# Kernel tuning notes

Hardware: AMD Instinct MI355X
Metric: run time of the kernel (lower is better)

The kernel has to match this reference:

```python
import jax, jax.numpy as jnp
import numpy as np

N, F, H = 22, 448, 64
LN_EPS = 1e-5


def _layernorm(h, g, b):
    mu = h.mean(axis=-1, keepdims=True)
    var = ((h - mu) ** 2).mean(axis=-1, keepdims=True)
    return (h - mu) / jnp.sqrt(var + LN_EPS) * g + b


def setup_inputs() -> dict:
    key = jax.random.key(0)
    ks = jax.random.split(key, 16)
    B = 128
    x = jax.random.normal(ks[0], (B, N, F), dtype=jnp.float32)
    s = lambda fan_in: 1.0 / np.sqrt(fan_in)
    # correlation-branch edge_weight_net: Linear(2F,64) -> ReLU -> Linear(64,1) -> Sigmoid
    cw1 = jax.random.uniform(ks[1], (2 * F, 64), jnp.float32, -s(2 * F), s(2 * F))
    cb1 = jax.random.uniform(ks[2], (64,), jnp.float32, -s(2 * F), s(2 * F))
    cw2 = jax.random.uniform(ks[3], (64, 1), jnp.float32, -s(64), s(64))
    cb2 = jax.random.uniform(ks[4], (1,), jnp.float32, -s(64), s(64))
    # semantic branch
    emb = jax.random.normal(ks[5], (N, H), dtype=jnp.float32) * 0.01
    D = 2 * H + 2 * F
    sw1 = jax.random.uniform(ks[6], (D, H), jnp.float32, -s(D), s(D))
    sb1 = jax.random.uniform(ks[7], (H,), jnp.float32, -s(D), s(D))
    ln_g = jnp.ones((H,), jnp.float32)
    ln_b = jnp.zeros((H,), jnp.float32)
    sw2 = jax.random.uniform(ks[8], (H, H // 2), jnp.float32, -s(H), s(H))
    sb2 = jax.random.uniform(ks[9], (H // 2,), jnp.float32, -s(H), s(H))
    sw3 = jax.random.uniform(ks[10], (H // 2, 1), jnp.float32, -s(H // 2), s(H // 2))
    sb3 = jax.random.uniform(ks[11], (1,), jnp.float32, -s(H // 2), s(H // 2))
    thr = jnp.asarray(0.3, jnp.float32)
    alpha_p = jnp.asarray(0.6, jnp.float32)
    return dict(x=x, cw1=cw1, cb1=cb1, cw2=cw2, cb2=cb2, emb=emb,
                sw1=sw1, sb1=sb1, ln_g=ln_g, ln_b=ln_b,
                sw2=sw2, sb2=sb2, sw3=sw3, sb3=sb3,
                thr=thr, alpha_p=alpha_p)


def reference(x, cw1, cb1, cw2, cb2, emb, sw1, sb1, ln_g, ln_b,
              sw2, sb2, sw3, sb3, thr, alpha_p):
    B, n, f = x.shape
    eye = jnp.eye(n, dtype=x.dtype)[None]

    # ---- Correlation graph ----
    xc = x - x.mean(axis=-1, keepdims=True)
    std = jnp.std(x, axis=-1, ddof=1, keepdims=True) + 1e-8  # torch std is unbiased
    xn = xc / std
    corr = jnp.abs(jnp.einsum('bif,bjf->bij', xn, xn) / f)
    # pairwise edge features (B,N,N,2F)
    xi = jnp.broadcast_to(x[:, :, None, :], (B, n, n, f))
    xj = jnp.broadcast_to(x[:, None, :, :], (B, n, n, f))
    ef = jnp.concatenate([xi, xj], axis=-1)
    h = jax.nn.relu(ef @ cw1 + cb1)
    w_corr = jax.nn.sigmoid((h @ cw2 + cb2)[..., 0])
    g_corr = corr * w_corr + eye

    # ---- Semantic graph ----
    ei = jnp.broadcast_to(emb[None, :, None, :], (B, n, n, H))
    ej = jnp.broadcast_to(emb[None, None, :, :], (B, n, n, H))
    sf = jnp.concatenate([ei, ej, xi, xj], axis=-1)  # (B,N,N,2H+2F)
    h1 = jax.nn.relu(_layernorm(sf @ sw1 + sb1, ln_g, ln_b))
    h2 = jax.nn.relu(h1 @ sw2 + sb2)
    w_sem = jax.nn.sigmoid((h2 @ sw3 + sb3)[..., 0])  # (B,N,N)
    # original loop fills only i<j and mirrors; diagonal stays 0
    upper = jnp.triu(w_sem, k=1)
    adj = upper + jnp.swapaxes(upper, 1, 2)
    t = jax.nn.sigmoid(thr)
    adj = jnp.where(adj > t, adj, jnp.zeros_like(adj))
    g_sem = adj + eye

    # ---- Learned fusion ----
    alpha = jax.nn.sigmoid(alpha_p)
    return alpha * g_corr + (1.0 - alpha) * g_sem
```

## Files before the change

kernel.cpp:

```cpp
#include <hip/hip_runtime.h>
#include <math.h>

namespace {
constexpr int kN = 22;
constexpr int kF = 448;
constexpr int kNP = kN * kN;
constexpr int kXStr = 452;
constexpr int kSm1 = kN * kXStr + 2 * kN;
constexpr int kAStr = 68;
constexpr int kBStr = 68;
constexpr int kPStr = 68;
constexpr int kVStr = 68;
}

__global__ __launch_bounds__(256) void hgc_k1(
    const float* __restrict__ x,
    const float* __restrict__ cw1, const float* __restrict__ cb1,
    const float* __restrict__ emb,
    const float* __restrict__ sw1, const float* __restrict__ sb1,
    float* __restrict__ C, float* __restrict__ g,
    int M, int Mtiles, int nGemm)
{
    __shared__ __align__(16) float sm[kSm1];
    const int tid = threadIdx.x;

    if ((int)blockIdx.x < nGemm) {
        float* As = sm;
        float* Bs = sm + 64 * kAStr;
        const int bm = blockIdx.x % Mtiles;
        const int bn = blockIdx.x / Mtiles;
        const int m0 = bm * 64;

        const float* Wsrc =
            (bn == 0) ? cw1 :
            (bn == 1) ? cw1 + 448 * 64 :
            (bn == 2) ? sw1 + 128 * 64 :
                        sw1 + 576 * 64;

        const int tm = tid & 15;
        const int tn = tid >> 4;
        const int ld_row = tid >> 4;
        const int ld_kq  = tid & 15;

        float acc[4][4];
        #pragma unroll
        for (int i = 0; i < 4; ++i)
            #pragma unroll
            for (int j = 0; j < 4; ++j) acc[i][j] = 0.f;

        float4 rA[4], rB[4];
        #pragma unroll
        for (int p = 0; p < 4; ++p) {
            const int row = ld_row + p * 16;
            int m = m0 + row; if (m >= M) m = M - 1;
            rA[p] = *(const float4*)&x[(size_t)m * kF + ld_kq * 4];
            rB[p] = *(const float4*)&Wsrc[(size_t)row * 64 + ld_kq * 4];
        }

        for (int k0 = 0; k0 < kF; k0 += 64) {
            #pragma unroll
            for (int p = 0; p < 4; ++p) {
                const int row = ld_row + p * 16;
                As[(ld_kq * 4 + 0) * kAStr + row] = rA[p].x;
                As[(ld_kq * 4 + 1) * kAStr + row] = rA[p].y;
                As[(ld_kq * 4 + 2) * kAStr + row] = rA[p].z;
                As[(ld_kq * 4 + 3) * kAStr + row] = rA[p].w;
                *(float4*)&Bs[row * kBStr + ld_kq * 4] = rB[p];
            }
            __syncthreads();
            const int kn = k0 + 64;
            if (kn < kF) {
                #pragma unroll
                for (int p = 0; p < 4; ++p) {
                    const int row = ld_row + p * 16;
                    int m = m0 + row; if (m >= M) m = M - 1;
                    rA[p] = *(const float4*)&x[(size_t)m * kF + kn + ld_kq * 4];
                    rB[p] = *(const float4*)&Wsrc[(size_t)(kn + row) * 64 + ld_kq * 4];
                }
            } else if (bn >= 2) {
                const float* W2 = sw1 + (bn == 2 ? 0 : 64) * 64;
                #pragma unroll
                for (int p = 0; p < 4; ++p) {
                    const int row = ld_row + p * 16;
                    const int r = (m0 + row) % kN;
                    rA[p] = *(const float4*)&emb[(size_t)r * 64 + ld_kq * 4];
                    rB[p] = *(const float4*)&W2[(size_t)row * 64 + ld_kq * 4];
                }
            }
            #pragma unroll 8
            for (int k = 0; k < 64; ++k) {
                const float4 a4 = *(const float4*)&As[k * kAStr + tm * 4];
                const float4 b4 = *(const float4*)&Bs[k * kBStr + tn * 4];
                acc[0][0] = fmaf(a4.x, b4.x, acc[0][0]); acc[0][1] = fmaf(a4.x, b4.y, acc[0][1]);
                acc[0][2] = fmaf(a4.x, b4.z, acc[0][2]); acc[0][3] = fmaf(a4.x, b4.w, acc[0][3]);
                acc[1][0] = fmaf(a4.y, b4.x, acc[1][0]); acc[1][1] = fmaf(a4.y, b4.y, acc[1][1]);
                acc[1][2] = fmaf(a4.y, b4.z, acc[1][2]); acc[1][3] = fmaf(a4.y, b4.w, acc[1][3]);
                acc[2][0] = fmaf(a4.z, b4.x, acc[2][0]); acc[2][1] = fmaf(a4.z, b4.y, acc[2][1]);
                acc[2][2] = fmaf(a4.z, b4.z, acc[2][2]); acc[2][3] = fmaf(a4.z, b4.w, acc[2][3]);
                acc[3][0] = fmaf(a4.w, b4.x, acc[3][0]); acc[3][1] = fmaf(a4.w, b4.y, acc[3][1]);
                acc[3][2] = fmaf(a4.w, b4.z, acc[3][2]); acc[3][3] = fmaf(a4.w, b4.w, acc[3][3]);
            }
            __syncthreads();
        }

        if (bn >= 2) {
            #pragma unroll
            for (int p = 0; p < 4; ++p) {
                const int row = ld_row + p * 16;
                As[(ld_kq * 4 + 0) * kAStr + row] = rA[p].x;
                As[(ld_kq * 4 + 1) * kAStr + row] = rA[p].y;
                As[(ld_kq * 4 + 2) * kAStr + row] = rA[p].z;
                As[(ld_kq * 4 + 3) * kAStr + row] = rA[p].w;
                *(float4*)&Bs[row * kBStr + ld_kq * 4] = rB[p];
            }
            __syncthreads();
            #pragma unroll 8
            for (int k = 0; k < 64; ++k) {
                const float4 a4 = *(const float4*)&As[k * kAStr + tm * 4];
                const float4 b4 = *(const float4*)&Bs[k * kBStr + tn * 4];
                acc[0][0] = fmaf(a4.x, b4.x, acc[0][0]); acc[0][1] = fmaf(a4.x, b4.y, acc[0][1]);
                acc[0][2] = fmaf(a4.x, b4.z, acc[0][2]); acc[0][3] = fmaf(a4.x, b4.w, acc[0][3]);
                acc[1][0] = fmaf(a4.y, b4.x, acc[1][0]); acc[1][1] = fmaf(a4.y, b4.y, acc[1][1]);
                acc[1][2] = fmaf(a4.y, b4.z, acc[1][2]); acc[1][3] = fmaf(a4.y, b4.w, acc[1][3]);
                acc[2][0] = fmaf(a4.z, b4.x, acc[2][0]); acc[2][1] = fmaf(a4.z, b4.y, acc[2][1]);
                acc[2][2] = fmaf(a4.z, b4.z, acc[2][2]); acc[2][3] = fmaf(a4.z, b4.w, acc[2][3]);
                acc[3][0] = fmaf(a4.w, b4.x, acc[3][0]); acc[3][1] = fmaf(a4.w, b4.y, acc[3][1]);
                acc[3][2] = fmaf(a4.w, b4.z, acc[3][2]); acc[3][3] = fmaf(a4.w, b4.w, acc[3][3]);
            }
        }

        float4 bias = {0, 0, 0, 0};
        if (bn == 0)      bias = *(const float4*)&cb1[tn * 4];
        else if (bn == 2) bias = *(const float4*)&sb1[tn * 4];
        #pragma unroll
        for (int i = 0; i < 4; ++i) {
            const int m = m0 + tm * 4 + i;
            if (m < M) {
                float4 o;
                o.x = acc[i][0] + bias.x; o.y = acc[i][1] + bias.y;
                o.z = acc[i][2] + bias.z; o.w = acc[i][3] + bias.w;
                *(float4*)&C[(size_t)m * 256 + bn * 64 + tn * 4] = o;
            }
        }
    } else {
        float* smu = sm + kN * kXStr;
        float* sis = smu + kN;
        const int b = blockIdx.x - nGemm;

        const float4* xb4 = (const float4*)(x + (size_t)b * (kN * kF));
        for (int idx = tid; idx < kN * kF / 4; idx += 256) {
            const float4 v = xb4[idx];
            const int r = idx / 112;
            const int k = (idx - r * 112) * 4;
            float* d = sm + r * kXStr + k;
            d[0] = v.x; d[1] = v.y; d[2] = v.z; d[3] = v.w;
        }
        __syncthreads();

        {
            const int wid = tid >> 6, lane = tid & 63;
            for (int r = wid; r < kN; r += 4) {
                const float* row = sm + r * kXStr;
                float s = 0.f;
                #pragma unroll
                for (int c = 0; c < 7; ++c) s += row[c * 64 + lane];
                #pragma unroll
                for (int o = 32; o; o >>= 1) s += __shfl_xor(s, o, 64);
                const float mean = s * (1.f / 448.f);
                float ss = 0.f;
                #pragma unroll
                for (int c = 0; c < 7; ++c) { const float d = row[c * 64 + lane] - mean; ss = fmaf(d, d, ss); }
                #pragma unroll
                for (int o = 32; o; o >>= 1) ss += __shfl_xor(ss, o, 64);
                if (lane == 0) {
                    smu[r] = mean;
                    sis[r] = 1.f / (sqrtf(ss * (1.f / 447.f)) + 1e-8f);
                }
            }
        }
        __syncthreads();

        if (tid < 253) {
            int rem = tid, i = 0;
            while (rem >= kN - i) { rem -= kN - i; ++i; }
            const int j = i + rem;
            const float4* ri = (const float4*)(sm + i * kXStr);
            const float4* rj = (const float4*)(sm + j * kXStr);
            float dot = 0.f;
            for (int q = 0; q < 112; ++q) {
                const float4 a = ri[q], bq = rj[q];
                dot = fmaf(a.x, bq.x, dot); dot = fmaf(a.y, bq.y, dot);
                dot = fmaf(a.z, bq.z, dot); dot = fmaf(a.w, bq.w, dot);
            }
            const float c = (dot - 448.f * smu[i] * smu[j]) * sis[i] * sis[j] * (1.f / 448.f);
            const float ac = fabsf(c);
            g[(size_t)b * kNP + i * 22 + j] = ac;
            g[(size_t)b * kNP + j * 22 + i] = ac;
        }
    }
}

__global__ __launch_bounds__(256) void hgc_k2(
    const float* __restrict__ C, const float* __restrict__ g,
    const float* __restrict__ cw2, const float* __restrict__ cb2,
    const float* __restrict__ sw2, const float* __restrict__ sb2,
    const float* __restrict__ sw3, const float* __restrict__ sb3,
    const float* __restrict__ ln_g, const float* __restrict__ ln_b,
    const float* __restrict__ thr, const float* __restrict__ alpha_p,
    float* __restrict__ out)
{
    __shared__ __align__(16) float sp[4 * kN * kPStr];
    __shared__ float sg[kNP];
    __shared__ __align__(16) float sw2s[2048];
    __shared__ float scw2[64], slng[64], slnb[64], ssw3[32], ssb2[32];
    __shared__ __align__(16) float vbuf[32 * kVStr];

    const int tid = threadIdx.x;
    const int b   = blockIdx.x >> 1;
    const int pb  = blockIdx.x & 1;

    #pragma unroll
    for (int a = 0; a < 4; ++a) {
        float* dst = sp + a * kN * kPStr;
        for (int idx = tid; idx < 352; idx += 256) {
            const int r = idx >> 4, kq = idx & 15;
            const float4 v = *(const float4*)&C[((size_t)(b * 22 + r)) * 256 + a * 64 + kq * 4];
            *(float4*)&dst[r * kPStr + kq * 4] = v;
        }
    }
    for (int idx = tid; idx < kNP; idx += 256) sg[idx] = g[(size_t)b * kNP + idx];
    {
        const float4* s4 = (const float4*)sw2;
        for (int idx = tid; idx < 512; idx += 256)
            *((float4*)(sw2s + idx * 4)) = s4[idx];
    }
    if (tid < 64)       { scw2[tid] = cw2[tid]; slng[tid] = ln_g[tid]; slnb[tid] = ln_b[tid]; }
    else if (tid < 96)  { ssw3[tid - 64] = sw3[tid - 64]; }
    else if (tid < 128) { ssb2[tid - 96] = sb2[tid - 96]; }
    __syncthreads();

    const int pl = tid >> 3;
    const int t  = tid & 7;
    const float* sa1 = sp;
    const float* sa2 = sp + kN * kPStr;
    const float* su1 = sp + 2 * kN * kPStr;
    const float* su2 = sp + 3 * kN * kPStr;

    for (int ch = 0; ch < 4; ++ch) {
        const int s_  = pb * 128 + ch * 32 + pl;
        const bool valid = s_ < 253;
        const int s = valid ? s_ : 252;
        int i, j;
        if (s < 231) {
            int rem = s, i0 = 0;
            while (rem >= 21 - i0) { rem -= 21 - i0; ++i0; }
            i = i0; j = i0 + 1 + rem;
        } else { i = j = s - 231; }

        float zc1 = 0.f, zc2 = 0.f;
        {
            const float* a1i = sa1 + i * kPStr + t * 8;
            const float* a2j = sa2 + j * kPStr + t * 8;
            const float* a1j = sa1 + j * kPStr + t * 8;
            const float* a2i = sa2 + i * kPStr + t * 8;
            const float4 i0 = *(const float4*)a1i, i1 = *(const float4*)(a1i + 4);
            const float4 j0 = *(const float4*)a2j, j1 = *(const float4*)(a2j + 4);
            const float4 k0 = *(const float4*)a1j, k1 = *(const float4*)(a1j + 4);
            const float4 l0 = *(const float4*)a2i, l1 = *(const float4*)(a2i + 4);
            const float4 w0 = *(const float4*)(scw2 + t * 8);
            const float4 w1 = *(const float4*)(scw2 + t * 8 + 4);
            zc1 = fmaf(fmaxf(i0.x + j0.x, 0.f), w0.x, zc1);
            zc1 = fmaf(fmaxf(i0.y + j0.y, 0.f), w0.y, zc1);
            zc1 = fmaf(fmaxf(i0.z + j0.z, 0.f), w0.z, zc1);
            zc1 = fmaf(fmaxf(i0.w + j0.w, 0.f), w0.w, zc1);
            zc1 = fmaf(fmaxf(i1.x + j1.x, 0.f), w1.x, zc1);
            zc1 = fmaf(fmaxf(i1.y + j1.y, 0.f), w1.y, zc1);
            zc1 = fmaf(fmaxf(i1.z + j1.z, 0.f), w1.z, zc1);
            zc1 = fmaf(fmaxf(i1.w + j1.w, 0.f), w1.w, zc1);
            zc2 = fmaf(fmaxf(k0.x + l0.x, 0.f), w0.x, zc2);
            zc2 = fmaf(fmaxf(k0.y + l0.y, 0.f), w0.y, zc2);
            zc2 = fmaf(fmaxf(k0.z + l0.z, 0.f), w0.z, zc2);
            zc2 = fmaf(fmaxf(k0.w + l0.w, 0.f), w0.w, zc2);
            zc2 = fmaf(fmaxf(k1.x + l1.x, 0.f), w1.x, zc2);
            zc2 = fmaf(fmaxf(k1.y + l1.y, 0.f), w1.y, zc2);
            zc2 = fmaf(fmaxf(k1.z + l1.z, 0.f), w1.z, zc2);
            zc2 = fmaf(fmaxf(k1.w + l1.w, 0.f), w1.w, zc2);
            zc1 += __shfl_xor(zc1, 1, 64); zc1 += __shfl_xor(zc1, 2, 64); zc1 += __shfl_xor(zc1, 4, 64);
            zc2 += __shfl_xor(zc2, 1, 64); zc2 += __shfl_xor(zc2, 2, 64); zc2 += __shfl_xor(zc2, 4, 64);
        }

        float raw[8];
        float s1 = 0.f;
        {
            const float* pu1 = su1 + i * kPStr + t * 8;
            const float* pu2 = su2 + j * kPStr + t * 8;
            const float4 u0 = *(const float4*)pu1, u1v = *(const float4*)(pu1 + 4);
            const float4 v0 = *(const float4*)pu2, v1v = *(const float4*)(pu2 + 4);
            raw[0] = u0.x + v0.x; raw[1] = u0.y + v0.y; raw[2] = u0.z + v0.z; raw[3] = u0.w + v0.w;
            raw[4] = u1v.x + v1v.x; raw[5] = u1v.y + v1v.y; raw[6] = u1v.z + v1v.z; raw[7] = u1v.w + v1v.w;
            #pragma unroll
            for (int c = 0; c < 8; ++c) s1 += raw[c];
        }
        s1 += __shfl_xor(s1, 1, 64); s1 += __shfl_xor(s1, 2, 64); s1 += __shfl_xor(s1, 4, 64);
        const float mean = s1 * (1.f / 64.f);
        float s2 = 0.f;
        #pragma unroll
        for (int c = 0; c < 8; ++c) { const float d = raw[c] - mean; s2 = fmaf(d, d, s2); }
        s2 += __shfl_xor(s2, 1, 64); s2 += __shfl_xor(s2, 2, 64); s2 += __shfl_xor(s2, 4, 64);
        const float rstd = rsqrtf(s2 * (1.f / 64.f) + 1e-5f);
        {
            float* vb = vbuf + pl * kVStr + t * 8;
            float4 o0, o1;
            o0.x = fmaxf(fmaf((raw[0] - mean) * rstd, slng[t*8+0], slnb[t*8+0]), 0.f);
            o0.y = fmaxf(fmaf((raw[1] - mean) * rstd, slng[t*8+1], slnb[t*8+1]), 0.f);
            o0.z = fmaxf(fmaf((raw[2] - mean) * rstd, slng[t*8+2], slnb[t*8+2]), 0.f);
            o0.w = fmaxf(fmaf((raw[3] - mean) * rstd, slng[t*8+3], slnb[t*8+3]), 0.f);
            o1.x = fmaxf(fmaf((raw[4] - mean) * rstd, slng[t*8+4], slnb[t*8+4]), 0.f);
            o1.y = fmaxf(fmaf((raw[5] - mean) * rstd, slng[t*8+5], slnb[t*8+5]), 0.f);
            o1.z = fmaxf(fmaf((raw[6] - mean) * rstd, slng[t*8+6], slnb[t*8+6]), 0.f);
            o1.w = fmaxf(fmaf((raw[7] - mean) * rstd, slng[t*8+7], slnb[t*8+7]), 0.f);
            *(float4*)vb = o0;
            *(float4*)(vb + 4) = o1;
        }
        __syncthreads();

        float4 acc = {0, 0, 0, 0};
        {
            const float* vb = vbuf + pl * kVStr;
            for (int k = 0; k < 64; ++k) {
                const float v = vb[k];
                const float4 w = *((const float4*)(sw2s + k * 32 + t * 4));
                acc.x = fmaf(v, w.x, acc.x); acc.y = fmaf(v, w.y, acc.y);
                acc.z = fmaf(v, w.z, acc.z); acc.w = fmaf(v, w.w, acc.w);
            }
        }
        float z2;
        {
            const int o0 = t * 4;
            z2  = fmaxf(acc.x + ssb2[o0 + 0], 0.f) * ssw3[o0 + 0];
            z2 += fmaxf(acc.y + ssb2[o0 + 1], 0.f) * ssw3[o0 + 1];
            z2 += fmaxf(acc.z + ssb2[o0 + 2], 0.f) * ssw3[o0 + 2];
            z2 += fmaxf(acc.w + ssb2[o0 + 3], 0.f) * ssw3[o0 + 3];
            z2 += __shfl_xor(z2, 1, 64); z2 += __shfl_xor(z2, 2, 64); z2 += __shfl_xor(z2, 4, 64);
        }

        if (valid && t == 0) {
            const float alpha = 1.f / (1.f + __expf(-alpha_p[0]));
            const float wc_ij = 1.f / (1.f + __expf(-(zc1 + cb2[0])));
            float gsem;
            if (i == j) {
                gsem = 1.f;
            } else {
                const float wsem = 1.f / (1.f + expf(-(z2 + sb3[0])));
                const float tt   = 1.f / (1.f + expf(-thr[0]));
                gsem = (wsem > tt) ? wsem : 0.f;
            }
            const float gc_ij = fmaf(sg[i * 22 + j], wc_ij, (i == j) ? 1.f : 0.f);
            out[(size_t)b * kNP + i * 22 + j] = fmaf(alpha, gc_ij, (1.f - alpha) * gsem);
            if (i != j) {
                const float wc_ji = 1.f / (1.f + __expf(-(zc2 + cb2[0])));
                const float gc_ji = sg[j * 22 + i] * wc_ji;
                out[(size_t)b * kNP + j * 22 + i] = fmaf(alpha, gc_ji, (1.f - alpha) * gsem);
            }
        }
        __syncthreads();
    }
}

extern "C" void kernel_launch(void* const* d_in, const int* in_sizes, int n_in,
                              void* d_out, int out_size, void* d_ws, size_t ws_size,
                              hipStream_t stream)
{
    (void)n_in; (void)out_size; (void)ws_size;
    const float* x     = (const float*)d_in[0];
    const float* cw1   = (const float*)d_in[1];
    const float* cb1   = (const float*)d_in[2];
    const float* cw2   = (const float*)d_in[3];
    const float* cb2   = (const float*)d_in[4];
    const float* emb   = (const float*)d_in[5];
    const float* sw1   = (const float*)d_in[6];
    const float* sb1   = (const float*)d_in[7];
    const float* ln_g  = (const float*)d_in[8];
    const float* ln_b  = (const float*)d_in[9];
    const float* sw2   = (const float*)d_in[10];
    const float* sb2   = (const float*)d_in[11];
    const float* sw3   = (const float*)d_in[12];
    const float* sb3   = (const float*)d_in[13];
    const float* thr   = (const float*)d_in[14];
    const float* alpha = (const float*)d_in[15];
    float* out = (float*)d_out;
    float* ws  = (float*)d_ws;

    const int B = in_sizes[0] / (kN * kF);
    const int M = kN * B;
    const int Mtiles = (M + 63) / 64;
    const int nGemm = Mtiles * 4;

    float* C = ws;
    float* g = ws + (size_t)M * 256;

    hipLaunchKernelGGL(hgc_k1, dim3(nGemm + B), dim3(256), 0, stream,
                       x, cw1, cb1, emb, sw1, sb1, C, g, M, Mtiles, nGemm);
    hipLaunchKernelGGL(hgc_k2, dim3(2 * B), dim3(256), 0, stream,
                       C, g, cw2, cb2, sw2, sb2, sw3, sb3, ln_g, ln_b, thr, alpha, out);
}
```

Before: 135.1 us.

## Halve GEMM tile rows and split corr and pair kernels across more blocks

The GEMM tile in the first kernel shrinks from 64 to 32 rows, so each thread computes 2x4 outputs and twice as many blocks are launched. The correlation branch is split into two blocks per batch, each handling 11 rows and computing every (i,j) entry directly instead of mirroring. The second kernel is split into four blocks per batch, each processing two chunks of pairs. The aim is more blocks to fill the GPU's compute units, at the cost of less data reuse per tile, repeated loading of x in the correlation blocks, and duplicated dot products.

```diff
diff --git a/kernel.cpp b/kernel.cpp
--- a/kernel.cpp
+++ b/kernel.cpp
@@ -4,13 +4,23 @@
 namespace {
 constexpr int kN = 22;
 constexpr int kF = 448;
-constexpr int kNP = kN * kN;
+constexpr int kNP = 484;
 constexpr int kXStr = 452;
 constexpr int kSm1 = kN * kXStr + 2 * kN;
-constexpr int kAStr = 68;
+constexpr int kAStr = 36;
 constexpr int kBStr = 68;
 constexpr int kPStr = 68;
 constexpr int kVStr = 68;
+
+__device__ __forceinline__ void map_slot(int s, int& i, int& j) {
+    if (s < 231) {
+        int rem = s, i0 = 0;
+        while (rem >= 21 - i0) { rem -= 21 - i0; ++i0; }
+        i = i0; j = i0 + 1 + rem;
+    } else {
+        i = j = s - 231;
+    }
+}
 }
 
 __global__ __launch_bounds__(256) void hgc_k1(
@@ -29,7 +39,7 @@
         float* Bs = sm + 64 * kAStr;
         const int bm = blockIdx.x % Mtiles;
         const int bn = blockIdx.x / Mtiles;
-        const int m0 = bm * 64;
+        const int m0 = bm * 32;
 
         const float* Wsrc =
             (bn == 0) ? cw1 :
@@ -39,102 +49,99 @@
 
         const int tm = tid & 15;
         const int tn = tid >> 4;
-        const int ld_row = tid >> 4;
-        const int ld_kq  = tid & 15;
-
-        float acc[4][4];
+        float acc[2][4];
         #pragma unroll
-        for (int i = 0; i < 4; ++i)
+        for (int i = 0; i < 2; ++i)
             #pragma unroll
             for (int j = 0; j < 4; ++j) acc[i][j] = 0.f;
 
-        float4 rA[4], rB[4];
-        #pragma unroll
-        for (int p = 0; p < 4; ++p) {
-            const int row = ld_row + p * 16;
-            int m = m0 + row; if (m >= M) m = M - 1;
-            rA[p] = *(const float4*)&x[(size_t)m * kF + ld_kq * 4];
-            rB[p] = *(const float4*)&Wsrc[(size_t)row * 64 + ld_kq * 4];
-        }
-
-        for (int k0 = 0; k0 < kF; k0 += 64) {
+        float4 rA[2], rB[4];
+
+        auto preMain = [&](int k0) {
+            #pragma unroll
+            for (int p = 0; p < 2; ++p) {
+                const int idx = tid + p * 256;
+                const int row = idx >> 4, kq = idx & 15;
+                int m = m0 + row; if (m >= M) m = M - 1;
+                rA[p] = *(const float4*)&x[(size_t)m * kF + k0 + kq * 4];
+            }
             #pragma unroll
             for (int p = 0; p < 4; ++p) {
-                const int row = ld_row + p * 16;
-                As[(ld_kq * 4 + 0) * kAStr + row] = rA[p].x;
-                As[(ld_kq * 4 + 1) * kAStr + row] = rA[p].y;
-                As[(ld_kq * 4 + 2) * kAStr + row] = rA[p].z;
-                As[(ld_kq * 4 + 3) * kAStr + row] = rA[p].w;
-                *(float4*)&Bs[row * kBStr + ld_kq * 4] = rB[p];
-            }
-            __syncthreads();
-            const int kn = k0 + 64;
-            if (kn < kF) {
-                #pragma unroll
-                for (int p = 0; p < 4; ++p) {
-                    const int row = ld_row + p * 16;
-                    int m = m0 + row; if (m >= M) m = M - 1;
-                    rA[p] = *(const float4*)&x[(size_t)m * kF + kn + ld_kq * 4];
-                    rB[p] = *(const float4*)&Wsrc[(size_t)(kn + row) * 64 + ld_kq * 4];
-                }
-            } else if (bn >= 2) {
-                const float* W2 = sw1 + (bn == 2 ? 0 : 64) * 64;
-                #pragma unroll
-                for (int p = 0; p < 4; ++p) {
-                    const int row = ld_row + p * 16;
-                    const int r = (m0 + row) % kN;
-                    rA[p] = *(const float4*)&emb[(size_t)r * 64 + ld_kq * 4];
-                    rB[p] = *(const float4*)&W2[(size_t)row * 64 + ld_kq * 4];
-                }
-            }
+                const int idx = tid + p * 256;
+                const int k = idx >> 4, nq = idx & 15;
+                rB[p] = *(const float4*)&Wsrc[(size_t)(k0 + k) * 64 + nq * 4];
+            }
+        };
+        auto preEmb = [&]() {
+            const float* W2 = sw1 + (bn == 2 ? 0 : 64) * 64;
+            #pragma unroll
+            for (int p = 0; p < 2; ++p) {
+                const int idx = tid + p * 256;
+                const int row = idx >> 4, kq = idx & 15;
+                const int r = (m0 + row) % kN;
+                rA[p] = *(const float4*)&emb[(size_t)r * 64 + kq * 4];
+            }
+            #pragma unroll
+            for (int p = 0; p < 4; ++p) {
+                const int idx = tid + p * 256;
+                const int k = idx >> 4, nq = idx & 15;
+                rB[p] = *(const float4*)&W2[(size_t)k * 64 + nq * 4];
+            }
+        };
+        auto commit = [&]() {
+            #pragma unroll
+            for (int p = 0; p < 2; ++p) {
+                const int idx = tid + p * 256;
+                const int row = idx >> 4, kq = idx & 15;
+                As[(kq * 4 + 0) * kAStr + row] = rA[p].x;
+                As[(kq * 4 + 1) * kAStr + row] = rA[p].y;
+                As[(kq * 4 + 2) * kAStr + row] = rA[p].z;
+                As[(kq * 4 + 3) * kAStr + row] = rA[p].w;
+            }
+            #pragma unroll
+            for (int p = 0; p < 4; ++p) {
+                const int idx = tid + p * 256;
+                const int k = idx >> 4, nq = idx & 15;
+                *(float4*)&Bs[k * kBStr + nq * 4] = rB[p];
+            }
+        };
+        auto compute = [&]() {
             #pragma unroll 8
             for (int k = 0; k < 64; ++k) {
-                const float4 a4 = *(const float4*)&As[k * kAStr + tm * 4];
+                const float2 a2 = *(const float2*)&As[k * kAStr + tm * 2];
                 const float4 b4 = *(const float4*)&Bs[k * kBStr + tn * 4];
-                acc[0][0] = fmaf(a4.x, b4.x, acc[0][0]); acc[0][1] = fmaf(a4.x, b4.y, acc[0][1]);
-                acc[0][2] = fmaf(a4.x, b4.z, acc[0][2]); acc[0][3] = fmaf(a4.x, b4.w, acc[0][3]);
-                acc[1][0] = fmaf(a4.y, b4.x, acc[1][0]); acc[1][1] = fmaf(a4.y, b4.y, acc[1][1]);
-                acc[1][2] = fmaf(a4.y, b4.z, acc[1][2]); acc[1][3] = fmaf(a4.y, b4.w, acc[1][3]);
-                acc[2][0] = fmaf(a4.z, b4.x, acc[2][0]); acc[2][1] = fmaf(a4.z, b4.y, acc[2][1]);
-                acc[2][2] = fmaf(a4.z, b4.z, acc[2][2]); acc[2][3] = fmaf(a4.z, b4.w, acc[2][3]);
-                acc[3][0] = fmaf(a4.w, b4.x, acc[3][0]); acc[3][1] = fmaf(a4.w, b4.y, acc[3][1]);
-                acc[3][2] = fmaf(a4.w, b4.z, acc[3][2]); acc[3][3] = fmaf(a4.w, b4.w, acc[3][3]);
-            }
+                acc[0][0] = fmaf(a2.x, b4.x, acc[0][0]);
+                acc[0][1] = fmaf(a2.x, b4.y, acc[0][1]);
+                acc[0][2] = fmaf(a2.x, b4.z, acc[0][2]);
+                acc[0][3] = fmaf(a2.x, b4.w, acc[0][3]);
+                acc[1][0] = fmaf(a2.y, b4.x, acc[1][0]);
+                acc[1][1] = fmaf(a2.y, b4.y, acc[1][1]);
+                acc[1][2] = fmaf(a2.y, b4.z, acc[1][2]);
+                acc[1][3] = fmaf(a2.y, b4.w, acc[1][3]);
+            }
+        };
+
+        preMain(0);
+        commit();
+        __syncthreads();
+        for (int c = 0; c < 7; ++c) {
+            if (c < 6) preMain((c + 1) * 64);
+            else if (bn >= 2) preEmb();
+            compute();
             __syncthreads();
-        }
-
-        if (bn >= 2) {
-            #pragma unroll
-            for (int p = 0; p < 4; ++p) {
-                const int row = ld_row + p * 16;
-                As[(ld_kq * 4 + 0) * kAStr + row] = rA[p].x;
-                As[(ld_kq * 4 + 1) * kAStr + row] = rA[p].y;
-                As[(ld_kq * 4 + 2) * kAStr + row] = rA[p].z;
-                As[(ld_kq * 4 + 3) * kAStr + row] = rA[p].w;
-                *(float4*)&Bs[row * kBStr + ld_kq * 4] = rB[p];
-            }
-            __syncthreads();
-            #pragma unroll 8
-            for (int k = 0; k < 64; ++k) {
-                const float4 a4 = *(const float4*)&As[k * kAStr + tm * 4];
-                const float4 b4 = *(const float4*)&Bs[k * kBStr + tn * 4];
-                acc[0][0] = fmaf(a4.x, b4.x, acc[0][0]); acc[0][1] = fmaf(a4.x, b4.y, acc[0][1]);
-                acc[0][2] = fmaf(a4.x, b4.z, acc[0][2]); acc[0][3] = fmaf(a4.x, b4.w, acc[0][3]);
-                acc[1][0] = fmaf(a4.y, b4.x, acc[1][0]); acc[1][1] = fmaf(a4.y, b4.y, acc[1][1]);
-                acc[1][2] = fmaf(a4.y, b4.z, acc[1][2]); acc[1][3] = fmaf(a4.y, b4.w, acc[1][3]);
-                acc[2][0] = fmaf(a4.z, b4.x, acc[2][0]); acc[2][1] = fmaf(a4.z, b4.y, acc[2][1]);
-                acc[2][2] = fmaf(a4.z, b4.z, acc[2][2]); acc[2][3] = fmaf(a4.z, b4.w, acc[2][3]);
-                acc[3][0] = fmaf(a4.w, b4.x, acc[3][0]); acc[3][1] = fmaf(a4.w, b4.y, acc[3][1]);
-                acc[3][2] = fmaf(a4.w, b4.z, acc[3][2]); acc[3][3] = fmaf(a4.w, b4.w, acc[3][3]);
-            }
-        }
+            if (c < 6 || bn >= 2) {
+                commit();
+                __syncthreads();
+            }
+        }
+        if (bn >= 2) compute();
 
         float4 bias = {0, 0, 0, 0};
         if (bn == 0)      bias = *(const float4*)&cb1[tn * 4];
         else if (bn == 2) bias = *(const float4*)&sb1[tn * 4];
         #pragma unroll
-        for (int i = 0; i < 4; ++i) {
-            const int m = m0 + tm * 4 + i;
+        for (int i = 0; i < 2; ++i) {
+            const int m = m0 + tm * 2 + i;
             if (m < M) {
                 float4 o;
                 o.x = acc[i][0] + bias.x; o.y = acc[i][1] + bias.y;
@@ -145,7 +152,9 @@
     } else {
         float* smu = sm + kN * kXStr;
         float* sis = smu + kN;
-        const int b = blockIdx.x - nGemm;
+        const int cb = blockIdx.x - nGemm;
+        const int b = cb >> 1;
+        const int r0 = (cb & 1) * 11;
 
         const float4* xb4 = (const float4*)(x + (size_t)b * (kN * kF));
         for (int idx = tid; idx < kN * kF / 4; idx += 256) {
@@ -180,10 +189,9 @@
         }
         __syncthreads();
 
-        if (tid < 253) {
-            int rem = tid, i = 0;
-            while (rem >= kN - i) { rem -= kN - i; ++i; }
-            const int j = i + rem;
+        for (int p = tid; p < 11 * kN; p += 256) {
+            const int pi = p / 22;
+            const int i = r0 + pi, j = p - pi * 22;
             const float4* ri = (const float4*)(sm + i * kXStr);
             const float4* rj = (const float4*)(sm + j * kXStr);
             float dot = 0.f;
@@ -193,9 +201,7 @@
                 dot = fmaf(a.z, bq.z, dot); dot = fmaf(a.w, bq.w, dot);
             }
             const float c = (dot - 448.f * smu[i] * smu[j]) * sis[i] * sis[j] * (1.f / 448.f);
-            const float ac = fabsf(c);
-            g[(size_t)b * kNP + i * 22 + j] = ac;
-            g[(size_t)b * kNP + j * 22 + i] = ac;
+            g[(size_t)b * kNP + i * 22 + j] = fabsf(c);
         }
     }
 }
@@ -216,8 +222,8 @@
     __shared__ __align__(16) float vbuf[32 * kVStr];
 
     const int tid = threadIdx.x;
-    const int b   = blockIdx.x >> 1;
-    const int pb  = blockIdx.x & 1;
+    const int b   = blockIdx.x >> 2;
+    const int pb  = blockIdx.x & 3;
 
     #pragma unroll
     for (int a = 0; a < 4; ++a) {
@@ -246,16 +252,11 @@
     const float* su1 = sp + 2 * kN * kPStr;
     const float* su2 = sp + 3 * kN * kPStr;
 
-    for (int ch = 0; ch < 4; ++ch) {
-        const int s_  = pb * 128 + ch * 32 + pl;
+    for (int ch = 0; ch < 2; ++ch) {
+        const int s_ = pb * 64 + ch * 32 + pl;
         const bool valid = s_ < 253;
         const int s = valid ? s_ : 252;
-        int i, j;
-        if (s < 231) {
-            int rem = s, i0 = 0;
-            while (rem >= 21 - i0) { rem -= 21 - i0; ++i0; }
-            i = i0; j = i0 + 1 + rem;
-        } else { i = j = s - 231; }
+        int i, j; map_slot(s, i, j);
 
         float zc1 = 0.f, zc2 = 0.f;
         {
@@ -346,7 +347,7 @@
 
         if (valid && t == 0) {
             const float alpha = 1.f / (1.f + __expf(-alpha_p[0]));
-            const float wc_ij = 1.f / (1.f + __expf(-(zc1 + cb2[0])));
+            const float wc1 = 1.f / (1.f + __expf(-(zc1 + cb2[0])));
             float gsem;
             if (i == j) {
                 gsem = 1.f;
@@ -355,12 +356,12 @@
                 const float tt   = 1.f / (1.f + expf(-thr[0]));
                 gsem = (wsem > tt) ? wsem : 0.f;
             }
-            const float gc_ij = fmaf(sg[i * 22 + j], wc_ij, (i == j) ? 1.f : 0.f);
-            out[(size_t)b * kNP + i * 22 + j] = fmaf(alpha, gc_ij, (1.f - alpha) * gsem);
+            const float gc1 = fmaf(sg[i * 22 + j], wc1, (i == j) ? 1.f : 0.f);
+            out[(size_t)b * kNP + i * 22 + j] = fmaf(alpha, gc1, (1.f - alpha) * gsem);
             if (i != j) {
-                const float wc_ji = 1.f / (1.f + __expf(-(zc2 + cb2[0])));
-                const float gc_ji = sg[j * 22 + i] * wc_ji;
-                out[(size_t)b * kNP + j * 22 + i] = fmaf(alpha, gc_ji, (1.f - alpha) * gsem);
+                const float wc2 = 1.f / (1.f + __expf(-(zc2 + cb2[0])));
+                const float gc2 = sg[j * 22 + i] * wc2;
+                out[(size_t)b * kNP + j * 22 + i] = fmaf(alpha, gc2, (1.f - alpha) * gsem);
             }
         }
         __syncthreads();
@@ -393,14 +394,14 @@
 
     const int B = in_sizes[0] / (kN * kF);
     const int M = kN * B;
-    const int Mtiles = (M + 63) / 64;
+    const int Mtiles = (M + 31) / 32;
     const int nGemm = Mtiles * 4;
 
     float* C = ws;
     float* g = ws + (size_t)M * 256;
 
-    hipLaunchKernelGGL(hgc_k1, dim3(nGemm + B), dim3(256), 0, stream,
+    hipLaunchKernelGGL(hgc_k1, dim3(nGemm + 2 * B), dim3(256), 0, stream,
                        x, cw1, cb1, emb, sw1, sb1, C, g, M, Mtiles, nGemm);
-    hipLaunchKernelGGL(hgc_k2, dim3(2 * B), dim3(256), 0, stream,
+    hipLaunchKernelGGL(hgc_k2, dim3(4 * B), dim3(256), 0, stream,
                        C, g, cw2, cb2, sw2, sb2, sw3, sb3, ln_g, ln_b, thr, alpha, out);
 }
```

Result: faster. 126.8 us (-6.2%).
